# Kernel tuning notes

Measured on AMD Instinct MI355X. Metric: run time of the kernel, lower is better.

Reference implementation:

```python
import jax, jax.numpy as jnp
import numpy as np

N = 100000   # nodes
E = 1600000  # edges
NF = 128     # nfeat
NH = 64      # nhid
NC = 16      # nclass
C = 1.0      # curvature
EPS = 1e-15
PROJ_EPS = 4e-3  # float32 boundary eps used by HGCN PoincareBall
SQC = C ** 0.5


def _norm(v):
    return jnp.maximum(jnp.linalg.norm(v, axis=-1, keepdims=True), EPS)


def _artanh(v):
    return jnp.arctanh(jnp.clip(v, -1.0 + 1e-7, 1.0 - 1e-7))


def proj(p):
    # clip to the open ball of radius (1-eps)/sqrt(c)
    n = _norm(p)
    maxnorm = (1.0 - PROJ_EPS) / SQC
    return jnp.where(n > maxnorm, p / n * maxnorm, p)


def expmap0(u):
    n = _norm(u)
    return jnp.tanh(SQC * n) * u / (SQC * n)


def logmap0(p):
    n = _norm(p)
    return _artanh(SQC * n) * p / (SQC * n)


def mobius_add(x, y):
    x2 = jnp.sum(x * x, axis=-1, keepdims=True)
    y2 = jnp.sum(y * y, axis=-1, keepdims=True)
    xy = jnp.sum(x * y, axis=-1, keepdims=True)
    num = (1.0 + 2.0 * C * xy + C * y2) * x + (1.0 - C * x2) * y
    den = 1.0 + 2.0 * C * xy + (C ** 2) * x2 * y2
    return num / jnp.maximum(den, EPS)


def mobius_matvec(W, p):
    # W: [out, in], p: [N, in] on the ball
    pn = _norm(p)
    mp = p @ W.T  # [N, out]
    mpn = jnp.linalg.norm(mp, axis=-1, keepdims=True)
    res = jnp.tanh(mpn / pn * _artanh(SQC * pn)) * mp / (SQC * jnp.maximum(mpn, EPS))
    return jnp.where(mpn <= EPS, jnp.zeros_like(res), res)


def setup_inputs() -> dict:
    key = jax.random.key(0)
    ks = jax.random.split(key, 16)
    inp = {
        "x": jax.random.normal(ks[0], (N, NF), dtype=jnp.float32),
        "src": jax.random.randint(ks[1], (E,), 0, N, dtype=jnp.int32),
        "dst": jax.random.randint(ks[2], (E,), 0, N, dtype=jnp.int32),
        "adj_val": jax.random.uniform(ks[3], (E,), dtype=jnp.float32) * 0.0625,
        "W1": jax.random.normal(ks[4], (NH, NF), dtype=jnp.float32) / np.sqrt(NF),
        "b1": jnp.zeros((NH,), dtype=jnp.float32),
        "W2": jax.random.normal(ks[5], (NH, NH), dtype=jnp.float32) / np.sqrt(NH),
        "b2": jnp.zeros((NH,), dtype=jnp.float32),
        "W3": jax.random.normal(ks[6], (NH, NH), dtype=jnp.float32) / np.sqrt(NH),
        "b3": jnp.zeros((NH,), dtype=jnp.float32),
        "W4": jax.random.normal(ks[7], (NH // 2, NH), dtype=jnp.float32) / np.sqrt(NH),
        "b4": jnp.zeros((NH // 2,), dtype=jnp.float32),
        "W5": jax.random.normal(ks[8], (NC, NH // 2), dtype=jnp.float32) / np.sqrt(NH // 2),
        "b5": jnp.zeros((NC,), dtype=jnp.float32),
    }
    return inp


def _hgc_layer(h, W, b, src, dst, adj_val):
    # HypLinear: mobius matvec + hyperbolic bias
    res = proj(mobius_matvec(W, h))
    hyp_b = proj(expmap0(b[None, :]))
    res = proj(mobius_add(res, hyp_b))
    # HypAgg: aggregate in tangent space at origin via sparse adj
    ht = logmap0(res)                                   # [N, d]
    msg = adj_val[:, None] * ht[src]                    # [E, d]
    agg = jax.ops.segment_sum(msg, dst, num_segments=N)  # [N, d]
    res = proj(expmap0(agg))
    # HypAct: relu in tangent space, re-map to ball
    res = proj(expmap0(jax.nn.relu(logmap0(res))))
    return res


def reference(x, src, dst, adj_val, W1, b1, W2, b2, W3, b3, W4, b4, W5, b5):
    h = proj(expmap0(x))  # map Euclidean features to the ball (proj_tan0 = identity)
    h = _hgc_layer(h, W1, b1, src, dst, adj_val)
    h = _hgc_layer(h, W2, b2, src, dst, adj_val)
    h = _hgc_layer(h, W3, b3, src, dst, adj_val)
    t = logmap0(h)  # back to tangent space for the Euclidean head
    z = jax.nn.relu(t @ W4.T + b4)
    return jax.nn.log_softmax(z @ W5.T + b5, axis=-1)  # [N, nclass]
```

## Files before the change

kernel.cpp:

```cpp
#include <hip/hip_runtime.h>
#include <hip/hip_fp16.h>
#include <math.h>

#define NFEAT 128
#define NHID  64
#define ATH996 3.106303f
#define CHUNK 4096
#define CAP   6144

typedef __attribute__((ext_vector_type(8))) _Float16 half8;
typedef __attribute__((ext_vector_type(4))) float floatx4;
typedef unsigned short ushort_t;
typedef unsigned long long u64;

__device__ __forceinline__ float wave_sum(float v) {
#pragma unroll
    for (int m = 1; m < 64; m <<= 1) v += __shfl_xor(v, m, 64);
    return v;
}

__device__ __forceinline__ float fast_tanh(float x) {
    float e = __expf(2.f * x);
    return 1.f - 2.f / (e + 1.f);
}

__device__ __forceinline__ float artanh_clip(float v) {
    const float lim = 0.99999988f;
    v = fminf(fmaxf(v, -lim), lim);
    return 0.5f * __logf((1.f + v) / (1.f - v));
}

__device__ __forceinline__ ushort_t f2h(float f) {
    __half h = __float2half(f);
    return *(ushort_t*)&h;
}

__device__ __forceinline__ unsigned pk2h(float a, float b) {
    return (unsigned)f2h(a) | ((unsigned)f2h(b) << 16);
}

__device__ __forceinline__ __half pe_adjh(unsigned p) {
    return __ushort_as_half((ushort_t)(p & 0x7fffu));
}

__global__ __launch_bounds__(256) void k_prep(
        const float* __restrict__ W1, const float* __restrict__ W2,
        const float* __restrict__ W3, const float* __restrict__ W4,
        const float* __restrict__ W5, const float* __restrict__ b1,
        const float* __restrict__ b2, const float* __restrict__ b3,
        ushort_t* __restrict__ Bpk1, ushort_t* __restrict__ Bpk2,
        ushort_t* __restrict__ Bpk3, ushort_t* __restrict__ Bpk4,
        ushort_t* __restrict__ Bpk5, float* __restrict__ hbs,
        float* __restrict__ hbns, int* __restrict__ gCur, int nb) {
    int bid = blockIdx.x, tid = threadIdx.x;
    if (bid >= 75) {
        for (int t = tid; t < nb; t += 256) gCur[t] = 0;
        return;
    }
    if (bid < 64) {
        const float* W; ushort_t* Bpk; int K, o;
        if (bid < 32)      { W = W1; Bpk = Bpk1; K = 128; o = bid * 256 + tid; }
        else if (bid < 48) { W = W2; Bpk = Bpk2; K = 64;  o = (bid - 32) * 256 + tid; }
        else               { W = W3; Bpk = Bpk3; K = 64;  o = (bid - 48) * 256 + tid; }
        int j = o & 7, c = (o >> 3) & 15, nf = (o >> 7) & 3, hi = (o >> 9) & 3,
            ks = o >> 11;
        Bpk[o] = f2h(W[(nf * 16 + c) * K + ks * 32 + hi * 8 + j]);
    } else if (bid < 72) {
        int o = (bid - 64) * 256 + tid;
        int j = o & 7, c = (o >> 3) & 15, nf = (o >> 7) & 1, hi = (o >> 8) & 3,
            ks = o >> 10;
        Bpk4[o] = f2h(W4[(nf * 16 + c) * 64 + ks * 32 + hi * 8 + j]);
    } else if (bid < 74) {
        int o = (bid - 72) * 256 + tid;
        if (o < 512) {
            int j = o & 7, c = (o >> 3) & 15, hi = o >> 7;
            Bpk5[o] = f2h(W5[c * 32 + hi * 8 + j]);
        }
    } else {
        if (tid < 192) {
            int wv = tid >> 6, lane = tid & 63;
            const float* b = (wv == 0) ? b1 : (wv == 1) ? b2 : b3;
            float bv = b[lane];
            float bn = fmaxf(sqrtf(wave_sum(bv * bv)), 1e-15f);
            float th = fast_tanh(bn);
            float f = th / bn;
            float hn = th;
            if (th > 0.996f) { f = 0.996f / bn; hn = 0.996f; }
            hbs[wv * 64 + lane] = bv * f;
            if (lane == 0) hbns[wv] = hn;
        }
    }
}

__device__ __forceinline__ void epi_vals(const float vin[4], float pn,
        float hbn, const float* __restrict__ hb, int c, float outv[4]) {
    float pp = 0.f;
#pragma unroll
    for (int nf = 0; nf < 4; ++nf) pp += vin[nf] * vin[nf];
#pragma unroll
    for (int m = 1; m < 16; m <<= 1) pp += __shfl_xor(pp, m, 64);
    float mpn = sqrtf(pp);
    float an = artanh_clip(pn);
    if (hbn <= 1e-15f) {
        float targ = (mpn / pn) * an;
        float scale = (targ > ATH996) ? (ATH996 / mpn) : (an / pn);
        if (mpn <= 1e-15f) scale = 0.f;
#pragma unroll
        for (int nf = 0; nf < 4; ++nf) outv[nf] = vin[nf] * scale;
    } else {
        float targ = (mpn / pn) * an;
        float th = fast_tanh(targ);
        float rn = fminf(th, 0.996f);
        float rs = (mpn <= 1e-15f) ? 0.f : (rn / mpn);
        float res[4], xyp = 0.f;
#pragma unroll
        for (int nf = 0; nf < 4; ++nf) {
            res[nf] = vin[nf] * rs;
            xyp += res[nf] * hb[nf * 16 + c];
        }
#pragma unroll
        for (int m = 1; m < 16; m <<= 1) xyp += __shfl_xor(xyp, m, 64);
        float x2 = rn * rn, y2 = hbn * hbn;
        float den = fmaxf(1.f + 2.f * xyp + x2 * y2, 1e-15f);
        float ca = (1.f + 2.f * xyp + y2) / den, cb = (1.f - x2) / den;
        float mv[4], mm = 0.f;
#pragma unroll
        for (int nf = 0; nf < 4; ++nf) {
            mv[nf] = ca * res[nf] + cb * hb[nf * 16 + c];
            mm += mv[nf] * mv[nf];
        }
#pragma unroll
        for (int m = 1; m < 16; m <<= 1) mm += __shfl_xor(mm, m, 64);
        float mn = sqrtf(mm);
        float mc = fminf(fmaxf(mn, 1e-15f), 0.996f);
        float msc = ((mn > 0.996f) ? (0.996f / mn) : 1.f) * artanh_clip(mc) / mc;
#pragma unroll
        for (int nf = 0; nf < 4; ++nf) outv[nf] = mv[nf] * msc;
    }
}

__global__ __launch_bounds__(256) void k_gemm1_scatter(
        const float* __restrict__ x, const ushort_t* __restrict__ Bpk,
        const float* __restrict__ hb, const float* __restrict__ hbn_p,
        ushort_t* __restrict__ htout, int n, int sortBlocks,
        const int* __restrict__ dst, const int* __restrict__ src,
        const float* __restrict__ adj, int* __restrict__ gCur,
        u64* __restrict__ gStage, int e, int nb) {
    __shared__ __align__(16) unsigned char smem[41984];
    int tid = threadIdx.x;
    if ((int)blockIdx.x < sortBlocks) {
        u64* stage   = (u64*)smem;
        int* cnt     = (int*)(smem + 32768);
        int* excl    = cnt + 512;
        int* rcnt    = excl + 512;
        int* myBase  = rcnt + 512;
        int* s       = myBase + 512;
        int start = blockIdx.x * CHUNK, end = min(e, start + CHUNK);
        for (int t = tid; t < nb; t += 256) { cnt[t] = 0; rcnt[t] = 0; }
        __syncthreads();
        for (int i = start + tid; i < end; i += 256)
            atomicAdd(&cnt[dst[i] >> 8], 1);
        __syncthreads();
        int v0 = (2 * tid < nb) ? cnt[2 * tid] : 0;
        int v1 = (2 * tid + 1 < nb) ? cnt[2 * tid + 1] : 0;
        int tsum = v0 + v1;
        s[tid] = tsum; __syncthreads();
        for (int o = 1; o < 256; o <<= 1) {
            int v = (tid >= o) ? s[tid - o] : 0;
            __syncthreads();
            s[tid] += v;
            __syncthreads();
        }
        int ex = s[tid] - tsum;
        if (2 * tid < nb) excl[2 * tid] = ex;
        if (2 * tid + 1 < nb) excl[2 * tid + 1] = ex + v0;
        __syncthreads();
        for (int t = tid; t < nb; t += 256)
            if (cnt[t]) myBase[t] = t * CAP + atomicAdd(&gCur[t], cnt[t]);
        for (int i = start + tid; i < end; i += 256) {
            int d = dst[i];
            int b = d >> 8;
            unsigned ab = (unsigned)__half_as_ushort(__float2half(adj[i])) & 0x7fffu;
            u64 u = ((u64)(unsigned)d << 32) |
                    (u64)(((unsigned)src[i] << 15) | ab);
            int r = atomicAdd(&rcnt[b], 1);
            stage[excl[b] + r] = u;
        }
        __syncthreads();
        int sz = end - start;
        for (int j = tid; j < sz; j += 256) {
            u64 u = stage[j];
            int b = (int)(u >> 40) & 0x1ff;
            gStage[myBase[b] + (j - excl[b])] = u;
        }
        return;
    }
    constexpr int RB = 256;
    unsigned char* As = smem;
    float* pns = (float*)(smem + 16384);
    float* fs  = pns + 64;
    int wv = tid >> 6, lane = tid & 63;
    int grp = lane >> 4, l = lane & 15;
    int rowBase = ((int)blockIdx.x - sortBlocks) * 64;
#pragma unroll
    for (int it = 0; it < 4; ++it) {
        int row = wv * 16 + it * 4 + grp, rg = rowBase + row;
        float4 va = make_float4(0.f, 0.f, 0.f, 0.f), vb = va;
        if (rg < n) {
            const float4* xr = (const float4*)(x + (size_t)rg * NFEAT + l * 8);
            va = xr[0]; vb = xr[1];
        }
        uint4 pk;
        pk.x = pk2h(va.x, va.y); pk.y = pk2h(va.z, va.w);
        pk.z = pk2h(vb.x, vb.y); pk.w = pk2h(vb.z, vb.w);
        unsigned byte = (unsigned)(row * RB + l * 16) ^ ((row & 7) << 4);
        *(uint4*)(As + byte) = pk;
        float ss = va.x * va.x + va.y * va.y + va.z * va.z + va.w * va.w +
                   vb.x * vb.x + vb.y * vb.y + vb.z * vb.z + vb.w * vb.w;
#pragma unroll
        for (int m = 1; m < 16; m <<= 1) ss += __shfl_xor(ss, m, 64);
        if (l == 0) {
            float nr = fmaxf(sqrtf(ss), 1e-15f);
            float th = fast_tanh(nr);
            float f = th / nr;
            float pn = fmaxf(th, 1e-15f);
            if (th > 0.996f) { f = 0.996f / nr; pn = 0.996f; }
            pns[row] = pn; fs[row] = f;
        }
    }
    int hi = lane >> 4, c = lane & 15;
    half8 bf[4][4];
#pragma unroll
    for (int ks = 0; ks < 4; ++ks)
#pragma unroll
        for (int nf = 0; nf < 4; ++nf)
            bf[ks][nf] = *(const half8*)(Bpk + (((size_t)(ks * 4 + hi) * 4 + nf) * 16 + c) * 8);
    floatx4 acc[4];
#pragma unroll
    for (int nf = 0; nf < 4; ++nf)
#pragma unroll
        for (int r = 0; r < 4; ++r) acc[nf][r] = 0.f;
    int arow = wv * 16 + c;
#pragma unroll
    for (int ks = 0; ks < 4; ++ks) {
        unsigned byte = (unsigned)(arow * RB + ks * 64 + hi * 16) ^ ((arow & 7) << 4);
        half8 af = *(const half8*)(As + byte);
#pragma unroll
        for (int nf = 0; nf < 4; ++nf)
            acc[nf] = __builtin_amdgcn_mfma_f32_16x16x32_f16(af, bf[ks][nf], acc[nf], 0, 0, 0);
    }
    float hbn = hbn_p[0];
#pragma unroll
    for (int r = 0; r < 4; ++r) {
        int row = wv * 16 + hi * 4 + r, rg = rowBase + row;
        float f = fs[row];
        float vin[4], outv[4];
#pragma unroll
        for (int nf = 0; nf < 4; ++nf) vin[nf] = acc[nf][r] * f;
        epi_vals(vin, pns[row], hbn, hb, c, outv);
        if (rg < n) {
#pragma unroll
            for (int nf = 0; nf < 4; ++nf)
                htout[(size_t)rg * 64 + nf * 16 + c] = f2h(outv[nf]);
        }
    }
}

__global__ __launch_bounds__(256) void k_bfinal(const u64* __restrict__ gStage,
        const int* __restrict__ gCur, int* __restrict__ off2,
        unsigned* __restrict__ pe, int n) {
    __shared__ int ncnt[256], nexcl[256], rcnt[256], s[256];
    int tid = threadIdx.x, b = blockIdx.x;
    int base = b * CAP;
    int ecnt = gCur[b];
    int nbeg = b << 8;
    ncnt[tid] = 0; rcnt[tid] = 0;
    __syncthreads();
    for (int j = tid; j < ecnt; j += 256) {
        int dl = ((int)(gStage[base + j] >> 32) & 0x1ffff) - nbeg;
        atomicAdd(&ncnt[dl], 1);
    }
    __syncthreads();
    int v = ncnt[tid];
    s[tid] = v; __syncthreads();
    for (int o = 1; o < 256; o <<= 1) {
        int t2 = (tid >= o) ? s[tid - o] : 0;
        __syncthreads();
        s[tid] += t2;
        __syncthreads();
    }
    nexcl[tid] = s[tid] - v;
    int node = nbeg + tid;
    if (node < n) {
        off2[2 * node]     = base + nexcl[tid];
        off2[2 * node + 1] = base + nexcl[tid] + v;
    }
    __syncthreads();
    for (int j = tid; j < ecnt; j += 256) {
        u64 u = gStage[base + j];
        int dl = ((int)(u >> 32) & 0x1ffff) - nbeg;
        int r = atomicAdd(&rcnt[dl], 1);
        pe[base + nexcl[dl] + r] = (unsigned)u;
    }
}

__global__ __launch_bounds__(256) void k_gemm64(
        const ushort_t* __restrict__ h, const float* __restrict__ nrm_in,
        const ushort_t* __restrict__ Bpk, const float* __restrict__ hb,
        const float* __restrict__ hbn_p, ushort_t* __restrict__ htout, int n) {
    constexpr int RB = 128;
    __shared__ __align__(16) unsigned char As[64 * RB];
    int tid = threadIdx.x, wv = tid >> 6, lane = tid & 63;
    int grp = lane >> 4, l = lane & 15;
    int rowBase = blockIdx.x * 64;
#pragma unroll
    for (int it = 0; it < 4; ++it) {
        int row = wv * 16 + it * 4 + grp, rg = rowBase + row;
        uint2 pk = make_uint2(0u, 0u);
        if (rg < n) pk = *(const uint2*)(h + (size_t)rg * 64 + l * 4);
        unsigned byte = (unsigned)(row * RB + l * 8) ^ ((row & 7) << 4);
        *(uint2*)(As + byte) = pk;
    }
    int hi = lane >> 4, c = lane & 15;
    half8 bf[2][4];
#pragma unroll
    for (int ks = 0; ks < 2; ++ks)
#pragma unroll
        for (int nf = 0; nf < 4; ++nf)
            bf[ks][nf] = *(const half8*)(Bpk + (((size_t)(ks * 4 + hi) * 4 + nf) * 16 + c) * 8);
    floatx4 acc[4];
#pragma unroll
    for (int nf = 0; nf < 4; ++nf)
#pragma unroll
        for (int r = 0; r < 4; ++r) acc[nf][r] = 0.f;
    int arow = wv * 16 + c;
#pragma unroll
    for (int ks = 0; ks < 2; ++ks) {
        unsigned byte = (unsigned)(arow * RB + ks * 64 + hi * 16) ^ ((arow & 7) << 4);
        half8 af = *(const half8*)(As + byte);
#pragma unroll
        for (int nf = 0; nf < 4; ++nf)
            acc[nf] = __builtin_amdgcn_mfma_f32_16x16x32_f16(af, bf[ks][nf], acc[nf], 0, 0, 0);
    }
    float hbn = hbn_p[0];
#pragma unroll
    for (int r = 0; r < 4; ++r) {
        int row = wv * 16 + hi * 4 + r, rg = rowBase + row;
        float pn = (rg < n) ? nrm_in[rg] : 1e-15f;
        float vin[4], outv[4];
#pragma unroll
        for (int nf = 0; nf < 4; ++nf) vin[nf] = acc[nf][r];
        epi_vals(vin, pn, hbn, hb, c, outv);
        if (rg < n) {
#pragma unroll
            for (int nf = 0; nf < 4; ++nf)
                htout[(size_t)rg * 64 + nf * 16 + c] = f2h(outv[nf]);
        }
    }
}

template <bool TANGENT_OUT>
__global__ __launch_bounds__(256) void k_agg_act(
        const ushort_t* __restrict__ ht, const int* __restrict__ off2,
        const unsigned* __restrict__ pe, ushort_t* __restrict__ hout,
        float* __restrict__ nrm_out, int n) {
    int tid = threadIdx.x;
    int grp = tid >> 4, l = tid & 15;
    int node = blockIdx.x * 16 + grp;
    if (node >= n) return;
    int beg = off2[2 * node], end = off2[2 * node + 1];
    const char* hb8 = (const char*)ht + l * 8;
    __half2 ax[4], ay[4];
#pragma unroll
    for (int u = 0; u < 4; ++u) {
        ax[u] = __float2half2_rn(0.f);
        ay[u] = __float2half2_rn(0.f);
    }
    int e = beg;
    for (; e + 7 < end; e += 8) {
        unsigned p[8];
#pragma unroll
        for (int u = 0; u < 8; ++u) p[u] = pe[e + u];
        uint2 rr[8];
#pragma unroll
        for (int u = 0; u < 8; ++u)
            rr[u] = *(const uint2*)(hb8 + ((size_t)(p[u] >> 15) << 7));
#pragma unroll
        for (int u = 0; u < 8; ++u) {
            __half2 w2 = __half2half2(pe_adjh(p[u]));
            ax[u & 3] = __hfma2(w2, *(__half2*)&rr[u].x, ax[u & 3]);
            ay[u & 3] = __hfma2(w2, *(__half2*)&rr[u].y, ay[u & 3]);
        }
    }
    for (; e < end; ++e) {
        unsigned p = pe[e];
        uint2 r = *(const uint2*)(hb8 + ((size_t)(p >> 15) << 7));
        __half2 w2 = __half2half2(pe_adjh(p));
        ax[0] = __hfma2(w2, *(__half2*)&r.x, ax[0]);
        ay[0] = __hfma2(w2, *(__half2*)&r.y, ay[0]);
    }
    float f0 = 0.f, f1 = 0.f, f2 = 0.f, f3 = 0.f;
#pragma unroll
    for (int u = 0; u < 4; ++u) {
        float2 vx = __half22float2(ax[u]);
        float2 vy = __half22float2(ay[u]);
        f0 += vx.x; f1 += vx.y; f2 += vy.x; f3 += vy.y;
    }
    float ss = f0 * f0 + f1 * f1 + f2 * f2 + f3 * f3;
#pragma unroll
    for (int m = 1; m < 16; m <<= 1) ss += __shfl_xor(ss, m, 64);
    float un = fmaxf(sqrtf(ss), 1e-15f);
    float thu = fast_tanh(un);
    float pf = thu / un, pn = thu;
    if (thu > 0.996f) { pf = 0.996f / un; pn = 0.996f; }
    float pnc = fmaxf(pn, 1e-15f);
    float ls = artanh_clip(pnc) / pnc * pf;
    float t0 = fmaxf(ls * f0, 0.f), t1 = fmaxf(ls * f1, 0.f);
    float t2 = fmaxf(ls * f2, 0.f), t3 = fmaxf(ls * f3, 0.f);
    float ss2 = t0 * t0 + t1 * t1 + t2 * t2 + t3 * t3;
#pragma unroll
    for (int m = 1; m < 16; m <<= 1) ss2 += __shfl_xor(ss2, m, 64);
    float tn = fmaxf(sqrtf(ss2), 1e-15f);
    uint2 ov;
    if (TANGENT_OUT) {
        float sc = (tn > ATH996) ? (ATH996 / tn) : 1.f;
        ov = make_uint2(pk2h(t0 * sc, t1 * sc), pk2h(t2 * sc, t3 * sc));
    } else {
        float tht = fast_tanh(tn);
        float rf = tht / tn, rn = tht;
        if (tht > 0.996f) { rf = 0.996f / tn; rn = 0.996f; }
        ov = make_uint2(pk2h(rf * t0, rf * t1), pk2h(rf * t2, rf * t3));
        if (l == 0) nrm_out[node] = fmaxf(rn, 1e-15f);
    }
    *(uint2*)((char*)hout + (size_t)node * 128 + l * 8) = ov;
}

__global__ __launch_bounds__(256) void k_head(
        const ushort_t* __restrict__ t_in, const ushort_t* __restrict__ Bpk4,
        const float* __restrict__ b4, const ushort_t* __restrict__ Bpk5,
        const float* __restrict__ b5, float* __restrict__ out, int n) {
    constexpr int RB = 128;
    __shared__ __align__(16) unsigned char As[64 * RB];
    __shared__ __align__(16) unsigned char Zs[4][16 * 80];
    int tid = threadIdx.x, wv = tid >> 6, lane = tid & 63;
    int grp = lane >> 4, l = lane & 15;
    int rowBase = blockIdx.x * 64;
#pragma unroll
    for (int it = 0; it < 4; ++it) {
        int row = wv * 16 + it * 4 + grp, rg = rowBase + row;
        uint2 pk = make_uint2(0u, 0u);
        if (rg < n) pk = *(const uint2*)(t_in + (size_t)rg * 64 + l * 4);
        unsigned byte = (unsigned)(row * RB + l * 8) ^ ((row & 7) << 4);
        *(uint2*)(As + byte) = pk;
    }
    int hi = lane >> 4, c = lane & 15;
    half8 bf4[2][2];
#pragma unroll
    for (int ks = 0; ks < 2; ++ks)
#pragma unroll
        for (int nf = 0; nf < 2; ++nf)
            bf4[ks][nf] = *(const half8*)(Bpk4 + (((size_t)(ks * 4 + hi) * 2 + nf) * 16 + c) * 8);
    floatx4 acc[2];
#pragma unroll
    for (int nf = 0; nf < 2; ++nf)
#pragma unroll
        for (int r = 0; r < 4; ++r) acc[nf][r] = 0.f;
    int arow = wv * 16 + c;
#pragma unroll
    for (int ks = 0; ks < 2; ++ks) {
        unsigned byte = (unsigned)(arow * RB + ks * 64 + hi * 16) ^ ((arow & 7) << 4);
        half8 af = *(const half8*)(As + byte);
#pragma unroll
        for (int nf = 0; nf < 2; ++nf)
            acc[nf] = __builtin_amdgcn_mfma_f32_16x16x32_f16(af, bf4[ks][nf], acc[nf], 0, 0, 0);
    }
    float bb0 = b4[c], bb1 = b4[16 + c];
#pragma unroll
    for (int r = 0; r < 4; ++r) {
        int zr = hi * 4 + r;
        *(ushort_t*)(Zs[wv] + zr * 80 + c * 2) = f2h(fmaxf(acc[0][r] + bb0, 0.f));
        *(ushort_t*)(Zs[wv] + zr * 80 + (16 + c) * 2) = f2h(fmaxf(acc[1][r] + bb1, 0.f));
    }
    half8 bf5 = *(const half8*)(Bpk5 + ((size_t)(hi * 16 + c)) * 8);
    half8 zf = *(const half8*)(Zs[wv] + c * 80 + hi * 16);
    floatx4 acc5;
#pragma unroll
    for (int r = 0; r < 4; ++r) acc5[r] = 0.f;
    acc5 = __builtin_amdgcn_mfma_f32_16x16x32_f16(zf, bf5, acc5, 0, 0, 0);
    float b5v = b5[c];
#pragma unroll
    for (int r = 0; r < 4; ++r) {
        float y = acc5[r] + b5v;
        float mx = y;
#pragma unroll
        for (int mk = 1; mk < 16; mk <<= 1) mx = fmaxf(mx, __shfl_xor(mx, mk, 64));
        float sm = __expf(y - mx);
#pragma unroll
        for (int mk = 1; mk < 16; mk <<= 1) sm += __shfl_xor(sm, mk, 64);
        int rg = rowBase + wv * 16 + hi * 4 + r;
        if (rg < n) out[(size_t)rg * 16 + c] = y - mx - __logf(sm);
    }
}

extern "C" void kernel_launch(void* const* d_in, const int* in_sizes, int n_in,
                              void* d_out, int out_size, void* d_ws, size_t ws_size,
                              hipStream_t stream) {
    const float* x   = (const float*)d_in[0];
    const int*   src = (const int*)d_in[1];
    const int*   dst = (const int*)d_in[2];
    const float* adj = (const float*)d_in[3];
    const float* W1  = (const float*)d_in[4];  const float* b1 = (const float*)d_in[5];
    const float* W2  = (const float*)d_in[6];  const float* b2 = (const float*)d_in[7];
    const float* W3  = (const float*)d_in[8];  const float* b3 = (const float*)d_in[9];
    const float* W4  = (const float*)d_in[10]; const float* b4 = (const float*)d_in[11];
    const float* W5  = (const float*)d_in[12]; const float* b5 = (const float*)d_in[13];
    float* out = (float*)d_out;

    const int N = in_sizes[0] / NFEAT;
    const int E = in_sizes[1];
    const int NB = (N + 255) >> 8;

    char* w = (char*)d_ws;
    auto alloc = [&](size_t bytes) {
        char* p = w; w += (bytes + 255) & ~(size_t)255; return p;
    };
    int* off2     = (int*)alloc((size_t)N * 2 * 4);
    int* gCur     = (int*)alloc((size_t)NB * 4);
    u64* gStage   = (u64*)alloc((size_t)NB * CAP * 8);
    unsigned* pe  = (unsigned*)alloc((size_t)NB * CAP * 4);
    ushort_t* B   = (ushort_t*)alloc((size_t)N * 64 * 2);
    ushort_t* D   = (ushort_t*)alloc((size_t)N * 64 * 2);
    float* nrm    = (float*)alloc((size_t)N * 4);
    float* hbs    = (float*)alloc(192 * 4);
    float* hbns   = (float*)alloc(4 * 4);
    ushort_t* Bpk1 = (ushort_t*)alloc(8192 * 2);
    ushort_t* Bpk2 = (ushort_t*)alloc(4096 * 2);
    ushort_t* Bpk3 = (ushort_t*)alloc(4096 * 2);
    ushort_t* Bpk4 = (ushort_t*)alloc(2048 * 2);
    ushort_t* Bpk5 = (ushort_t*)alloc(512 * 2);

    dim3 blk(256);
    int aggBlocks  = (N + 15) / 16;
    int gemmBlocks = (N + 63) / 64;
    int sortBlocks = (E + CHUNK - 1) / CHUNK;

    k_prep<<<76, blk, 0, stream>>>(W1, W2, W3, W4, W5, b1, b2, b3,
                                   Bpk1, Bpk2, Bpk3, Bpk4, Bpk5, hbs, hbns,
                                   gCur, NB);

    k_gemm1_scatter<<<sortBlocks + gemmBlocks, blk, 0, stream>>>(
        x, Bpk1, hbs, hbns, B, N, sortBlocks, dst, src, adj, gCur, gStage, E, NB);

    k_bfinal<<<NB, blk, 0, stream>>>(gStage, gCur, off2, pe, N);

    k_agg_act<false><<<aggBlocks, blk, 0, stream>>>(B, off2, pe, D, nrm, N);
    k_gemm64<<<gemmBlocks, blk, 0, stream>>>(D, nrm, Bpk2, hbs + 64, hbns + 1, B, N);
    k_agg_act<false><<<aggBlocks, blk, 0, stream>>>(B, off2, pe, D, nrm, N);
    k_gemm64<<<gemmBlocks, blk, 0, stream>>>(D, nrm, Bpk3, hbs + 128, hbns + 2, B, N);
    k_agg_act<true><<<aggBlocks, blk, 0, stream>>>(B, off2, pe, D, nullptr, N);

    k_head<<<gemmBlocks, blk, 0, stream>>>(D, Bpk4, b4, Bpk5, b5, out, N);
}
```

Before: 205.9 us.

## Split aggregation into column-quarter gather kernel and separate activation kernel

The fused gather-plus-activation kernel is split in two. A new k_aggq kernel gathers one 32-byte quarter of each neighbour row per block, with blocks interleaved so the eight consecutive blocks covering a pair of node tiles share the same edge lists, and writes the fp16 aggregate to a new buffer. A separate k_act kernel then does the norm, expmap, relu and logmap epilogue. The aim is to shrink the gathered working set per block so neighbour rows hit in cache more often, at the cost of reading the edge lists four times and an extra intermediate round trip plus three more launches.

```diff
diff --git a/kernel.cpp b/kernel.cpp
--- a/kernel.cpp
+++ b/kernel.cpp
@@ -359,17 +359,19 @@
     }
 }
 
-template <bool TANGENT_OUT>
-__global__ __launch_bounds__(256) void k_agg_act(
+__global__ __launch_bounds__(256) void k_aggq(
         const ushort_t* __restrict__ ht, const int* __restrict__ off2,
-        const unsigned* __restrict__ pe, ushort_t* __restrict__ hout,
-        float* __restrict__ nrm_out, int n) {
+        const unsigned* __restrict__ pe, ushort_t* __restrict__ aggout, int n) {
+    int xq = (int)blockIdx.x & 7;
+    int q = xq >> 1;
+    int tile = ((int)blockIdx.x >> 3) * 2 + (xq & 1);
     int tid = threadIdx.x;
-    int grp = tid >> 4, l = tid & 15;
-    int node = blockIdx.x * 16 + grp;
+    int l4 = tid & 3;
+    int node = tile * 64 + (tid >> 2);
     if (node >= n) return;
-    int beg = off2[2 * node], end = off2[2 * node + 1];
-    const char* hb8 = (const char*)ht + l * 8;
+    int2 be = *(const int2*)(off2 + 2 * node);
+    int beg = be.x, end = be.y;
+    const char* hb8 = (const char*)ht + q * 32 + l4 * 8;
     __half2 ax[4], ay[4];
 #pragma unroll
     for (int u = 0; u < 4; ++u) {
@@ -406,6 +408,22 @@
         float2 vy = __half22float2(ay[u]);
         f0 += vx.x; f1 += vx.y; f2 += vy.x; f3 += vy.y;
     }
+    uint2 ov = make_uint2(pk2h(f0, f1), pk2h(f2, f3));
+    *(uint2*)((char*)aggout + (size_t)node * 128 + q * 32 + l4 * 8) = ov;
+}
+
+template <bool TANGENT_OUT>
+__global__ __launch_bounds__(256) void k_act(
+        const ushort_t* __restrict__ agg, ushort_t* __restrict__ hout,
+        float* __restrict__ nrm_out, int n) {
+    int tid = threadIdx.x;
+    int grp = tid >> 4, l = tid & 15;
+    int node = blockIdx.x * 16 + grp;
+    if (node >= n) return;
+    uint2 v = *(const uint2*)((const char*)agg + (size_t)node * 128 + l * 8);
+    float2 vx = __half22float2(*(__half2*)&v.x);
+    float2 vy = __half22float2(*(__half2*)&v.y);
+    float f0 = vx.x, f1 = vx.y, f2 = vy.x, f3 = vy.y;
     float ss = f0 * f0 + f1 * f1 + f2 * f2 + f3 * f3;
 #pragma unroll
     for (int m = 1; m < 16; m <<= 1) ss += __shfl_xor(ss, m, 64);
@@ -530,6 +548,7 @@
     unsigned* pe  = (unsigned*)alloc((size_t)NB * CAP * 4);
     ushort_t* B   = (ushort_t*)alloc((size_t)N * 64 * 2);
     ushort_t* D   = (ushort_t*)alloc((size_t)N * 64 * 2);
+    ushort_t* AG  = (ushort_t*)alloc((size_t)N * 64 * 2);
     float* nrm    = (float*)alloc((size_t)N * 4);
     float* hbs    = (float*)alloc(192 * 4);
     float* hbns   = (float*)alloc(4 * 4);
@@ -540,9 +559,11 @@
     ushort_t* Bpk5 = (ushort_t*)alloc(512 * 2);
 
     dim3 blk(256);
-    int aggBlocks  = (N + 15) / 16;
+    int actBlocks  = (N + 15) / 16;
     int gemmBlocks = (N + 63) / 64;
     int sortBlocks = (E + CHUNK - 1) / CHUNK;
+    int tiles      = (N + 63) / 64;
+    int aggqBlocks = 8 * ((tiles + 1) / 2);
 
     k_prep<<<76, blk, 0, stream>>>(W1, W2, W3, W4, W5, b1, b2, b3,
                                    Bpk1, Bpk2, Bpk3, Bpk4, Bpk5, hbs, hbns,
@@ -553,11 +574,14 @@
 
     k_bfinal<<<NB, blk, 0, stream>>>(gStage, gCur, off2, pe, N);
 
-    k_agg_act<false><<<aggBlocks, blk, 0, stream>>>(B, off2, pe, D, nrm, N);
+    k_aggq<<<aggqBlocks, blk, 0, stream>>>(B, off2, pe, AG, N);
+    k_act<false><<<actBlocks, blk, 0, stream>>>(AG, D, nrm, N);
     k_gemm64<<<gemmBlocks, blk, 0, stream>>>(D, nrm, Bpk2, hbs + 64, hbns + 1, B, N);
-    k_agg_act<false><<<aggBlocks, blk, 0, stream>>>(B, off2, pe, D, nrm, N);
+    k_aggq<<<aggqBlocks, blk, 0, stream>>>(B, off2, pe, AG, N);
+    k_act<false><<<actBlocks, blk, 0, stream>>>(AG, D, nrm, N);
     k_gemm64<<<gemmBlocks, blk, 0, stream>>>(D, nrm, Bpk3, hbs + 128, hbns + 2, B, N);
-    k_agg_act<true><<<aggBlocks, blk, 0, stream>>>(B, off2, pe, D, nullptr, N);
+    k_aggq<<<aggqBlocks, blk, 0, stream>>>(B, off2, pe, AG, N);
+    k_act<true><<<actBlocks, blk, 0, stream>>>(AG, D, nullptr, N);
 
     k_head<<<gemmBlocks, blk, 0, stream>>>(D, Bpk4, b4, Bpk5, b5, out, N);
 }
```

Measured after the change: 407.7 us. 98.0% more time.
